# Kernel tuning notes

Measured on AMD Instinct MI355X. Metric: run time of the kernel, lower is better.

The kernel has to match this reference:

```python
import jax, jax.numpy as jnp
import numpy as np

EPS = 1e-5
H = 1024  # hidden_size
IN = 1024  # input_size
B = 4096


def _layer_norm(x, gamma, beta):
    mu = jnp.mean(x, axis=-1, keepdims=True)
    var = jnp.mean(jnp.square(x - mu), axis=-1, keepdims=True)
    return (x - mu) * jax.lax.rsqrt(var + EPS) * gamma + beta


def setup_inputs() -> dict:
    key = jax.random.key(0)
    ks = jax.random.split(key, 8)
    s_h = 1.0 / np.sqrt(H)
    s_x = 1.0 / np.sqrt(IN)
    return {
        "x": jax.random.normal(ks[0], (B, IN), dtype=jnp.float32),
        "h": jax.random.normal(ks[1], (B, H), dtype=jnp.float32),
        "c": jax.random.normal(ks[2], (B, H), dtype=jnp.float32),
        # hidden_lin: Linear(H, 4H) with bias; input_lin: Linear(IN, 4H) no bias
        "W_h": jax.random.uniform(ks[3], (H, 4 * H), jnp.float32, -s_h, s_h),
        "b_h": jax.random.uniform(ks[4], (4 * H,), jnp.float32, -s_h, s_h),
        "W_x": jax.random.uniform(ks[5], (IN, 4 * H), jnp.float32, -s_x, s_x),
        # 4 gate LayerNorms stacked [4,H], plus LayerNorm for c
        "ln_g": jnp.ones((4, H), jnp.float32),
        "ln_b": jnp.zeros((4, H), jnp.float32),
        "lnc_g": jnp.ones((H,), jnp.float32),
        "lnc_b": jnp.zeros((H,), jnp.float32),
    }


def reference(x, h, c, W_h, b_h, W_x, ln_g, ln_b, lnc_g, lnc_b):
    # ifgo = hidden_lin(h) + input_lin(x) : [B, 4H]
    ifgo = h @ W_h + b_h + x @ W_x
    ifgo = ifgo.reshape(x.shape[0], 4, H)  # [B, 4, H]
    ifgo = _layer_norm(ifgo, ln_g, ln_b)   # per-gate LayerNorm over last dim
    i, f, g, o = ifgo[:, 0], ifgo[:, 1], ifgo[:, 2], ifgo[:, 3]
    c_next = jax.nn.sigmoid(f) * c + jax.nn.sigmoid(i) * jnp.tanh(g)
    h_next = jax.nn.sigmoid(o) * jnp.tanh(_layer_norm(c_next, lnc_g, lnc_b))
    return (h_next, c_next)
```

## Files before the change

### kernel.cpp

```cpp
#include <hip/hip_runtime.h>

typedef short bf16x8 __attribute__((ext_vector_type(8)));
typedef unsigned short u16x8 __attribute__((ext_vector_type(8)));
typedef float f32x4  __attribute__((ext_vector_type(4)));

__device__ __forceinline__ float bf2f(unsigned short u) {
  union { unsigned int i; float f; } x; x.i = ((unsigned int)u) << 16; return x.f;
}
__device__ __forceinline__ unsigned short f2bf(float f) {
  union { float f; unsigned int i; } x; x.f = f;
  unsigned int r = x.i + 0x7fffu + ((x.i >> 16) & 1u);
  return (unsigned short)(r >> 16);
}
__device__ __forceinline__ float sigm(float v) { return 1.f / (1.f + __expf(-v)); }
__device__ __forceinline__ float tanh_(float v) { return 1.f - 2.f / (__expf(2.f * v) + 1.f); }
__device__ __forceinline__ int is_fp32(const void* lng) {
  return ((*(const unsigned int*)lng) & 0xFFFFu) == 0u;
}

#define AS1 __attribute__((address_space(1)))
#define AS3 __attribute__((address_space(3)))

__global__ __launch_bounds__(256) void prep_kernel(
    const void* __restrict__ h, const void* __restrict__ x,
    const void* __restrict__ Wh, const void* __restrict__ Wx,
    const void* __restrict__ lng,
    unsigned short* __restrict__ Ap, unsigned short* __restrict__ Wt)
{
  __shared__ __align__(16) unsigned short tkn[64][64];
  const int fp = is_fp32(lng);
  if (blockIdx.x < 4096) {
    const int row = blockIdx.x;
    const int col = threadIdx.x * 8;
    const void* src; int sc;
    if (col < 1024) { src = h; sc = col; } else { src = x; sc = col - 1024; }
    u16x8 o;
    if (fp) {
      const float* s = (const float*)src + (size_t)row * 1024 + sc;
      float4 a = *(const float4*)s;
      float4 b = *(const float4*)(s + 4);
      o[0] = f2bf(a.x); o[1] = f2bf(a.y); o[2] = f2bf(a.z); o[3] = f2bf(a.w);
      o[4] = f2bf(b.x); o[5] = f2bf(b.y); o[6] = f2bf(b.z); o[7] = f2bf(b.w);
    } else {
      o = *(const u16x8*)((const unsigned short*)src + (size_t)row * 1024 + sc);
    }
    *(u16x8*)(Ap + (size_t)row * 2048 + col) = o;
  } else {
    const int bid = blockIdx.x - 4096;
    const int n0 = (bid & 63) * 64;
    const int k0 = (bid >> 6) * 64;
    const int t = threadIdx.x;
    const void* src; int krow;
    if (k0 < 1024) { src = Wh; krow = k0; } else { src = Wx; krow = k0 - 1024; }
    if (fp) {
#pragma unroll
      for (int i = 0; i < 4; ++i) {
        const int k  = (t >> 4) + i * 16;
        const int n4 = (t & 15) * 4;
        float4 w = *(const float4*)((const float*)src + (size_t)(krow + k) * 4096 + n0 + n4);
        ushort4 u; u.x = f2bf(w.x); u.y = f2bf(w.y); u.z = f2bf(w.z); u.w = f2bf(w.w);
        *(ushort4*)&tkn[k][n4] = u;
      }
    } else {
#pragma unroll
      for (int i = 0; i < 2; ++i) {
        const int k  = (t >> 3) + i * 32;
        const int n8 = (t & 7) * 8;
        *(u16x8*)&tkn[k][n8] =
            *(const u16x8*)((const unsigned short*)src + (size_t)(krow + k) * 4096 + n0 + n8);
      }
    }
    __syncthreads();
#pragma unroll
    for (int i = 0; i < 2; ++i) {
      const int n  = (t >> 3) + i * 32;
      const int k8 = (t & 7) * 8;
      u16x8 o;
#pragma unroll
      for (int j = 0; j < 8; ++j) o[j] = tkn[k8 + j][n];
      *(u16x8*)(Wt + (size_t)(n0 + n) * 2048 + k0 + k8) = o;
    }
  }
}


#define BAR()   __builtin_amdgcn_s_barrier()
#define SBAR()  __builtin_amdgcn_sched_barrier(0)
#define LGKM0() { asm volatile("s_waitcnt lgkmcnt(0)" ::: "memory"); SBAR(); }
#define LGKM8() { asm volatile("s_waitcnt lgkmcnt(8)" ::: "memory"); }
#define VMW(N)  { asm volatile("s_waitcnt vmcnt(" #N ")" ::: "memory"); }

#define LOAD_A(DB, MH)                                                         \
  { const unsigned short* _ba = &As[DB][(MH)*128 + wr*64 + fr][0];             \
    _Pragma("unroll") for (int mi = 0; mi < 4; ++mi)                           \
      _Pragma("unroll") for (int kh = 0; kh < 2; ++kh)                         \
        a[mi][kh] = *(const bf16x8*)(_ba + mi*1024 + ((kh*4 + fq) ^ xk) * 8); }

#define LOAD_B(DB, NH)                                                         \
  { const unsigned short* _bb = &Bs[DB][(NH)*128 + wc*32 + fr][0];             \
    _Pragma("unroll") for (int ni = 0; ni < 2; ++ni)                           \
      _Pragma("unroll") for (int kh = 0; kh < 2; ++kh)                         \
        b[ni][kh] = *(const bf16x8*)(_bb + ni*1024 + ((kh*4 + fq) ^ xk) * 8); }

#define MFMA16(MH, NH)                                                         \
  { __builtin_amdgcn_s_setprio(1);                                             \
    _Pragma("unroll") for (int kh = 0; kh < 2; ++kh)                           \
      _Pragma("unroll") for (int mi = 0; mi < 4; ++mi)                         \
        _Pragma("unroll") for (int ni = 0; ni < 2; ++ni)                       \
          acc[MH][mi][NH][ni] = __builtin_amdgcn_mfma_f32_16x16x32_bf16(       \
              a[mi][kh], b[ni][kh], acc[MH][mi][NH][ni], 0, 0, 0);             \
    __builtin_amdgcn_s_setprio(0); }

#define STAGE(G, LDS, ROW0, H, KT)                                             \
  { _Pragma("unroll") for (int l = 0; l < 2; ++l) {                            \
      const int _idx = l * 512 + tid;                                          \
      const int _r = _idx >> 3;                                                \
      const int _sg = (_idx & 7) ^ (_r & 7);                                   \
      const unsigned short* _src = (G) + (size_t)((ROW0) + (H)*128 + _r) * 2048\
                                   + ((KT) << 6) + _sg * 8;                    \
      __builtin_amdgcn_global_load_lds((const AS1 void*)_src,                  \
          (AS3 void*)(&(LDS)[0][0] + (H)*8192 + (l*512 + wave*64)*8), 16, 0, 0);\
  } }

__global__ __launch_bounds__(512, 2) void gemm_kernel(
    const unsigned short* __restrict__ Ap,
    const unsigned short* __restrict__ Wt,
    unsigned short* __restrict__ Cout)
{
  __shared__ __align__(16) unsigned short As[2][256][64];
  __shared__ __align__(16) unsigned short Bs[2][256][64];

  const int bid = blockIdx.x;
  const int swz = (bid & 7) * 32 + (bid >> 3);
  const int bm = swz >> 4, bn = swz & 15;
  const int arow = bm * 256, brow = bn * 256;

  const int tid  = threadIdx.x;
  const int wave = tid >> 6, lane = tid & 63;
  const int wr = wave >> 2, wc = wave & 3;
  const int fr = lane & 15, fq = lane >> 4;
  const int xk = fr & 7;

  f32x4 acc[2][4][2][2] = {};
  bf16x8 a[4][2], b[2][2];

  STAGE(Ap, As[0], arow, 0, 0);
  STAGE(Ap, As[0], arow, 1, 0);
  STAGE(Wt, Bs[0], brow, 0, 0);
  STAGE(Wt, Bs[0], brow, 1, 0);
  STAGE(Ap, As[1], arow, 0, 1);
  STAGE(Wt, Bs[1], brow, 1, 1);
  VMW(4);
  SBAR(); BAR();

#pragma unroll 1
  for (int it = 0; it < 16; ++it) {
    const int t1 = (2 * it + 1) & 31;
    const int t2 = (2 * it + 2) & 31;
    const int t3 = (2 * it + 3) & 31;

    STAGE(Wt, Bs[1], brow, 0, t1);
    LOAD_A(0, 0) LOAD_B(0, 0)
    LGKM8();
    SBAR(); BAR(); LGKM0();
    MFMA16(0, 0);
    SBAR(); BAR();
    STAGE(Ap, As[1], arow, 1, t1);
    LOAD_B(0, 1)
    SBAR(); BAR(); LGKM0();
    MFMA16(0, 1);
    SBAR(); BAR();
    STAGE(Ap, As[0], arow, 0, t2);
    LOAD_A(0, 1)
    SBAR(); BAR(); LGKM0();
    MFMA16(1, 1);
    SBAR(); BAR();
    STAGE(Wt, Bs[0], brow, 1, t2);
    LOAD_B(0, 0)
    SBAR(); BAR(); LGKM0();
    MFMA16(1, 0);
    VMW(4);
    SBAR(); BAR();
    STAGE(Wt, Bs[0], brow, 0, t2);
    LOAD_A(1, 0) LOAD_B(1, 0)
    LGKM8();
    SBAR(); BAR(); LGKM0();
    MFMA16(0, 0);
    SBAR(); BAR();
    STAGE(Ap, As[0], arow, 1, t2);
    LOAD_B(1, 1)
    SBAR(); BAR(); LGKM0();
    MFMA16(0, 1);
    SBAR(); BAR();
    STAGE(Ap, As[1], arow, 0, t3);
    LOAD_A(1, 1)
    SBAR(); BAR(); LGKM0();
    MFMA16(1, 1);
    SBAR(); BAR();
    STAGE(Wt, Bs[1], brow, 1, t3);
    LOAD_B(1, 0)
    SBAR(); BAR(); LGKM0();
    MFMA16(1, 0);
    VMW(4);
    SBAR(); BAR();
  }
  VMW(0);

  unsigned short* Cb = Cout + (size_t)arow * 4096 + brow;
#pragma unroll
  for (int mh = 0; mh < 2; ++mh)
#pragma unroll
    for (int mi = 0; mi < 4; ++mi)
#pragma unroll
      for (int nh = 0; nh < 2; ++nh)
#pragma unroll
        for (int ni = 0; ni < 2; ++ni) {
          const int row = mh * 128 + wr * 64 + mi * 16 + fq * 4;
          const int col = nh * 128 + wc * 32 + ni * 16 + fr;
#pragma unroll
          for (int r = 0; r < 4; ++r)
            Cb[(size_t)(row + r) * 4096 + col] = f2bf(acc[mh][mi][nh][ni][r]);
        }
}

__device__ __forceinline__ float4 load4(const void* p, size_t idx, int fp) {
  if (fp) return *(const float4*)((const float*)p + idx);
  ushort4 u = *(const ushort4*)((const unsigned short*)p + idx);
  return make_float4(bf2f(u.x), bf2f(u.y), bf2f(u.z), bf2f(u.w));
}
__device__ __forceinline__ void store4(void* p, size_t idx, int fp,
                                       float a, float b, float c, float d) {
  if (fp) {
    *(float4*)((float*)p + idx) = make_float4(a, b, c, d);
  } else {
    ushort4 u; u.x = f2bf(a); u.y = f2bf(b); u.z = f2bf(c); u.w = f2bf(d);
    *(ushort4*)((unsigned short*)p + idx) = u;
  }
}

__global__ __launch_bounds__(256) void ln_lstm_kernel(
    const unsigned short* __restrict__ parts,
    const void* __restrict__ c,
    const void* __restrict__ bh,
    const void* __restrict__ ln_g,
    const void* __restrict__ ln_b,
    const void* __restrict__ lnc_g,
    const void* __restrict__ lnc_b,
    void* __restrict__ out)
{
  const int b = blockIdx.x;
  const int t = threadIdx.x;
  const int lane = t & 63, wave = t >> 6;
  const int fp = is_fp32(lnc_g);
  const unsigned short* P0 = parts + (size_t)b * 4096;

  __shared__ float sred[4][8];

  float v[4][4];
  float red[8];
#pragma unroll
  for (int q = 0; q < 4; ++q) {
    ushort4 p0 = *(const ushort4*)(P0 + q * 1024 + t * 4);
    float4 b4 = load4(bh, q * 1024 + t * 4, fp);
    v[q][0] = bf2f(p0.x) + b4.x;
    v[q][1] = bf2f(p0.y) + b4.y;
    v[q][2] = bf2f(p0.z) + b4.z;
    v[q][3] = bf2f(p0.w) + b4.w;
    red[q * 2]     = v[q][0] + v[q][1] + v[q][2] + v[q][3];
    red[q * 2 + 1] = v[q][0]*v[q][0] + v[q][1]*v[q][1] + v[q][2]*v[q][2] + v[q][3]*v[q][3];
  }
#pragma unroll
  for (int j = 0; j < 8; ++j) {
    float s = red[j];
#pragma unroll
    for (int off = 32; off > 0; off >>= 1) s += __shfl_down(s, off, 64);
    if (lane == 0) sred[wave][j] = s;
  }
  __syncthreads();
  float mu[4], rs[4];
#pragma unroll
  for (int q = 0; q < 4; ++q) {
    float s  = sred[0][2*q]   + sred[1][2*q]   + sred[2][2*q]   + sred[3][2*q];
    float sq = sred[0][2*q+1] + sred[1][2*q+1] + sred[2][2*q+1] + sred[3][2*q+1];
    mu[q] = s * (1.f / 1024.f);
    float var = sq * (1.f / 1024.f) - mu[q] * mu[q];
    rs[q] = rsqrtf(var + 1e-5f);
  }

  float4 gI = load4(ln_g, 0 * 1024 + t * 4, fp), bI = load4(ln_b, 0 * 1024 + t * 4, fp);
  float4 gF = load4(ln_g, 1 * 1024 + t * 4, fp), bF = load4(ln_b, 1 * 1024 + t * 4, fp);
  float4 gG = load4(ln_g, 2 * 1024 + t * 4, fp), bG = load4(ln_b, 2 * 1024 + t * 4, fp);
  float4 gO = load4(ln_g, 3 * 1024 + t * 4, fp), bO = load4(ln_b, 3 * 1024 + t * 4, fp);
  float gg[4][4] = { {gI.x,gI.y,gI.z,gI.w}, {gF.x,gF.y,gF.z,gF.w},
                     {gG.x,gG.y,gG.z,gG.w}, {gO.x,gO.y,gO.z,gO.w} };
  float gb[4][4] = { {bI.x,bI.y,bI.z,bI.w}, {bF.x,bF.y,bF.z,bF.w},
                     {bG.x,bG.y,bG.z,bG.w}, {bO.x,bO.y,bO.z,bO.w} };

  float4 c4 = load4(c, (size_t)b * 1024 + t * 4, fp);
  float cin[4] = { c4.x, c4.y, c4.z, c4.w };

  float cn[4], osg[4];
  float csum = 0.f, csq = 0.f;
#pragma unroll
  for (int e = 0; e < 4; ++e) {
    float iv = (v[0][e] - mu[0]) * rs[0] * gg[0][e] + gb[0][e];
    float fv = (v[1][e] - mu[1]) * rs[1] * gg[1][e] + gb[1][e];
    float gv = (v[2][e] - mu[2]) * rs[2] * gg[2][e] + gb[2][e];
    float ov = (v[3][e] - mu[3]) * rs[3] * gg[3][e] + gb[3][e];
    float cne = sigm(fv) * cin[e] + sigm(iv) * tanh_(gv);
    cn[e] = cne; csum += cne; csq += cne * cne;
    osg[e] = sigm(ov);
  }
  store4(out, (size_t)4096 * 1024 + (size_t)b * 1024 + t * 4, fp, cn[0], cn[1], cn[2], cn[3]);

  __syncthreads();
  {
    float s0 = csum, s1 = csq;
#pragma unroll
    for (int off = 32; off > 0; off >>= 1) { s0 += __shfl_down(s0, off, 64); s1 += __shfl_down(s1, off, 64); }
    if (lane == 0) { sred[wave][0] = s0; sred[wave][1] = s1; }
  }
  __syncthreads();
  float cs   = sred[0][0] + sred[1][0] + sred[2][0] + sred[3][0];
  float csq2 = sred[0][1] + sred[1][1] + sred[2][1] + sred[3][1];
  float mu_c = cs * (1.f / 1024.f);
  float var_c = csq2 * (1.f / 1024.f) - mu_c * mu_c;
  float rs_c = rsqrtf(var_c + 1e-5f);

  float4 cg4 = load4(lnc_g, t * 4, fp);
  float4 cb4 = load4(lnc_b, t * 4, fp);

  float hn[4];
  float cgv[4] = { cg4.x, cg4.y, cg4.z, cg4.w };
  float cbv[4] = { cb4.x, cb4.y, cb4.z, cb4.w };
#pragma unroll
  for (int e = 0; e < 4; ++e)
    hn[e] = osg[e] * tanh_((cn[e] - mu_c) * rs_c * cgv[e] + cbv[e]);
  store4(out, (size_t)b * 1024 + t * 4, fp, hn[0], hn[1], hn[2], hn[3]);
}

extern "C" void kernel_launch(void* const* d_in, const int* in_sizes, int n_in,
                              void* d_out, int out_size, void* d_ws, size_t ws_size,
                              hipStream_t stream) {
  const void* x    = d_in[0];
  const void* h    = d_in[1];
  const void* c    = d_in[2];
  const void* Wh   = d_in[3];
  const void* bh   = d_in[4];
  const void* Wx   = d_in[5];
  const void* lng  = d_in[6];
  const void* lnb  = d_in[7];
  const void* lncg = d_in[8];
  const void* lncb = d_in[9];

  char* ws = (char*)d_ws;
  unsigned short* parts = (unsigned short*)ws;
  unsigned short* Wt    = (unsigned short*)(ws + (size_t)64 * 1024 * 1024);
  unsigned short* Ap    = (unsigned short*)(ws + (size_t)80 * 1024 * 1024);

  prep_kernel<<<6144, 256, 0, stream>>>(h, x, Wh, Wx, lng, Ap, Wt);
  gemm_kernel<<<256, 512, 0, stream>>>(Ap, Wt, parts);
  ln_lstm_kernel<<<4096, 256, 0, stream>>>(parts, c, bh, lng, lnb, lncg, lncb, d_out);
}
```

Before: 227.0 us.

## Double-buffer B fragments in registers and reorder GEMM stage/load schedule

Adds a second register set for B fragments (bA/bB) so the next B tile can be read from LDS while MFMAs run on the current one. The global-to-LDS staging order and the vmcnt waits are rearranged: each sub-step now waits with vmcnt(8) instead of only once per half-iteration with vmcnt(4), and the first B fragment is preloaded before the loop. The aim is to overlap LDS reads with matrix math and spread memory waits more evenly. The cost is more VGPRs, which risks occupancy at launch bounds (512,2), and the changed wait and stage ordering could introduce read-before-ready hazards.

```diff
diff --git a/kernel.cpp b/kernel.cpp
--- a/kernel.cpp
+++ b/kernel.cpp
@@ -87,7 +87,6 @@
 #define BAR()   __builtin_amdgcn_s_barrier()
 #define SBAR()  __builtin_amdgcn_sched_barrier(0)
 #define LGKM0() { asm volatile("s_waitcnt lgkmcnt(0)" ::: "memory"); SBAR(); }
-#define LGKM8() { asm volatile("s_waitcnt lgkmcnt(8)" ::: "memory"); }
 #define VMW(N)  { asm volatile("s_waitcnt vmcnt(" #N ")" ::: "memory"); }
 
 #define LOAD_A(DB, MH)                                                         \
@@ -96,19 +95,19 @@
       _Pragma("unroll") for (int kh = 0; kh < 2; ++kh)                         \
         a[mi][kh] = *(const bf16x8*)(_ba + mi*1024 + ((kh*4 + fq) ^ xk) * 8); }
 
-#define LOAD_B(DB, NH)                                                         \
+#define LOAD_B(DB, NH, BT)                                                     \
   { const unsigned short* _bb = &Bs[DB][(NH)*128 + wc*32 + fr][0];             \
     _Pragma("unroll") for (int ni = 0; ni < 2; ++ni)                           \
       _Pragma("unroll") for (int kh = 0; kh < 2; ++kh)                         \
-        b[ni][kh] = *(const bf16x8*)(_bb + ni*1024 + ((kh*4 + fq) ^ xk) * 8); }
-
-#define MFMA16(MH, NH)                                                         \
+        (BT)[ni][kh] = *(const bf16x8*)(_bb + ni*1024 + ((kh*4 + fq) ^ xk) * 8); }
+
+#define MFMA16(MH, NH, BT)                                                     \
   { __builtin_amdgcn_s_setprio(1);                                             \
     _Pragma("unroll") for (int kh = 0; kh < 2; ++kh)                           \
       _Pragma("unroll") for (int mi = 0; mi < 4; ++mi)                         \
         _Pragma("unroll") for (int ni = 0; ni < 2; ++ni)                       \
           acc[MH][mi][NH][ni] = __builtin_amdgcn_mfma_f32_16x16x32_bf16(       \
-              a[mi][kh], b[ni][kh], acc[MH][mi][NH][ni], 0, 0, 0);             \
+              a[mi][kh], (BT)[ni][kh], acc[MH][mi][NH][ni], 0, 0, 0);          \
     __builtin_amdgcn_s_setprio(0); }
 
 #define STAGE(G, LDS, ROW0, H, KT)                                             \
@@ -142,16 +141,17 @@
   const int xk = fr & 7;
 
   f32x4 acc[2][4][2][2] = {};
-  bf16x8 a[4][2], b[2][2];
-
+  bf16x8 a[4][2], bA[2][2], bB[2][2];
+
+  STAGE(Wt, Bs[0], brow, 0, 0);
   STAGE(Ap, As[0], arow, 0, 0);
+  STAGE(Wt, Bs[0], brow, 1, 0);
   STAGE(Ap, As[0], arow, 1, 0);
-  STAGE(Wt, Bs[0], brow, 0, 0);
-  STAGE(Wt, Bs[0], brow, 1, 0);
+  STAGE(Wt, Bs[1], brow, 0, 1);
   STAGE(Ap, As[1], arow, 0, 1);
-  STAGE(Wt, Bs[1], brow, 1, 1);
   VMW(4);
   SBAR(); BAR();
+  LOAD_B(0, 0, bA)
 
 #pragma unroll 1
   for (int it = 0; it < 16; ++it) {
@@ -159,49 +159,53 @@
     const int t2 = (2 * it + 2) & 31;
     const int t3 = (2 * it + 3) & 31;
 
-    STAGE(Wt, Bs[1], brow, 0, t1);
-    LOAD_A(0, 0) LOAD_B(0, 0)
-    LGKM8();
-    SBAR(); BAR(); LGKM0();
-    MFMA16(0, 0);
+    STAGE(Wt, Bs[1], brow, 1, t1);
+    VMW(8);
+    LOAD_A(0, 0)
+    SBAR(); BAR(); LGKM0();
+    MFMA16(0, 0, bA);
     SBAR(); BAR();
     STAGE(Ap, As[1], arow, 1, t1);
-    LOAD_B(0, 1)
-    SBAR(); BAR(); LGKM0();
-    MFMA16(0, 1);
+    VMW(8);
+    LOAD_B(0, 1, bB)
+    SBAR(); BAR(); LGKM0();
+    MFMA16(0, 1, bB);
+    SBAR(); BAR();
+    STAGE(Wt, Bs[0], brow, 0, t2);
+    VMW(8);
+    LOAD_A(0, 1)
+    SBAR(); BAR(); LGKM0();
+    MFMA16(1, 1, bB);
     SBAR(); BAR();
     STAGE(Ap, As[0], arow, 0, t2);
-    LOAD_A(0, 1)
-    SBAR(); BAR(); LGKM0();
-    MFMA16(1, 1);
+    VMW(8);
+    LOAD_B(1, 0, bB)
+    SBAR(); BAR(); LGKM0();
+    MFMA16(1, 0, bA);
     SBAR(); BAR();
     STAGE(Wt, Bs[0], brow, 1, t2);
-    LOAD_B(0, 0)
-    SBAR(); BAR(); LGKM0();
-    MFMA16(1, 0);
-    VMW(4);
-    SBAR(); BAR();
-    STAGE(Wt, Bs[0], brow, 0, t2);
-    LOAD_A(1, 0) LOAD_B(1, 0)
-    LGKM8();
-    SBAR(); BAR(); LGKM0();
-    MFMA16(0, 0);
+    VMW(8);
+    LOAD_A(1, 0)
+    SBAR(); BAR(); LGKM0();
+    MFMA16(0, 0, bB);
     SBAR(); BAR();
     STAGE(Ap, As[0], arow, 1, t2);
-    LOAD_B(1, 1)
-    SBAR(); BAR(); LGKM0();
-    MFMA16(0, 1);
+    VMW(8);
+    LOAD_B(1, 1, bA)
+    SBAR(); BAR(); LGKM0();
+    MFMA16(0, 1, bA);
+    SBAR(); BAR();
+    STAGE(Wt, Bs[1], brow, 0, t3);
+    VMW(8);
+    LOAD_A(1, 1)
+    SBAR(); BAR(); LGKM0();
+    MFMA16(1, 1, bA);
     SBAR(); BAR();
     STAGE(Ap, As[1], arow, 0, t3);
-    LOAD_A(1, 1)
-    SBAR(); BAR(); LGKM0();
-    MFMA16(1, 1);
-    SBAR(); BAR();
-    STAGE(Wt, Bs[1], brow, 1, t3);
-    LOAD_B(1, 0)
-    SBAR(); BAR(); LGKM0();
-    MFMA16(1, 0);
-    VMW(4);
+    VMW(8);
+    LOAD_B(0, 0, bA)
+    SBAR(); BAR(); LGKM0();
+    MFMA16(1, 0, bB);
     SBAR(); BAR();
   }
   VMW(0);
```

New measurement: 221.8 us. -2.3%, faster.
